# Kernel tuning notes

Hardware: AMD Instinct MI355X
Metric: run time of the kernel (lower is better)

Reference implementation:

```python
import jax, jax.numpy as jnp
import numpy as np

WS = 8      # window size
S = 2       # num_heads
GRID = jnp.linspace(-2.0, 2.0, 8)  # RBF grid, num_grids=8
DENOM = 4.0 / 7.0                  # (grid_max-grid_min)/(num_grids-1)


def _layernorm(x, g, b, eps=1e-5):
    mu = x.mean(-1, keepdims=True)
    var = ((x - mu) ** 2).mean(-1, keepdims=True)
    return (x - mu) * jax.lax.rsqrt(var + eps) * g + b


def _fastkan(x, ln_g, ln_b, ws, wb, bb):
    # x: (..., in_dim). RBF basis: (..., in_dim, 8) -> flatten -> spline GEMM; plus SiLU base path.
    ln = _layernorm(x, ln_g, ln_b)
    basis = jnp.exp(-(((ln[..., None] - GRID) / DENOM) ** 2))
    flat = basis.reshape(*basis.shape[:-2], -1)
    return flat @ ws.T + jax.nn.silu(x) @ wb.T + bb


def setup_inputs() -> dict:
    key = jax.random.key(0)
    ks = jax.random.split(key, 16)
    d = {
        'x': jax.random.normal(ks[0], (4, 32, 256, 256), dtype=jnp.float32),
        'pn_g': jnp.ones((32,), jnp.float32), 'pn_b': jnp.zeros((32,), jnp.float32),
        'k1_ln_g': jnp.ones((16,), jnp.float32), 'k1_ln_b': jnp.zeros((16,), jnp.float32),
        'k1_ws': jax.random.normal(ks[1], (16, 128), jnp.float32) * 0.1,
        'k1_wb': jax.random.normal(ks[2], (16, 16), jnp.float32) * 0.1,
        'k1_bb': jnp.zeros((16,), jnp.float32),
        'k2_ln_g': jnp.ones((16,), jnp.float32), 'k2_ln_b': jnp.zeros((16,), jnp.float32),
        'k2_ws': jax.random.normal(ks[3], (16, 128), jnp.float32) * 0.1,
        'k2_wb': jax.random.normal(ks[4], (16, 16), jnp.float32) * 0.1,
        'k2_bb': jnp.zeros((16,), jnp.float32),
        'k3_ln_g': jnp.ones((32,), jnp.float32), 'k3_ln_b': jnp.zeros((32,), jnp.float32),
        'k3_ws': jax.random.normal(ks[5], (32, 256), jnp.float32) * 0.1,
        'k3_wb': jax.random.normal(ks[6], (32, 32), jnp.float32) * 0.1,
        'k3_bb': jnp.zeros((32,), jnp.float32),
        'k4_ln_g': jnp.ones((32,), jnp.float32), 'k4_ln_b': jnp.zeros((32,), jnp.float32),
        'k4_ws': jax.random.normal(ks[7], (32, 256), jnp.float32) * 0.1,
        'k4_wb': jax.random.normal(ks[8], (32, 32), jnp.float32) * 0.1,
        'k4_bb': jnp.zeros((32,), jnp.float32),
    }
    return d


def reference(x, pn_g, pn_b,
              k1_ln_g, k1_ln_b, k1_ws, k1_wb, k1_bb,
              k2_ln_g, k2_ln_b, k2_ws, k2_wb, k2_bb,
              k3_ln_g, k3_ln_b, k3_ws, k3_wb, k3_bb,
              k4_ln_g, k4_ln_b, k4_ws, k4_wb, k4_bb):
    B, C, H, W = x.shape
    c = C // S
    # b c h w -> b h w c, then window partition (shift_size=0, no padding)
    xh = jnp.transpose(x, (0, 2, 3, 1))
    wins = xh.reshape(B, H // WS, WS, W // WS, WS, C).transpose(0, 1, 3, 2, 4, 5).reshape(-1, WS, WS, C)
    b = wins.shape[0]
    # PreNormResidual
    y = _layernorm(wins, pn_g, pn_b)
    # branch 1: 'b h w (c s) -> b (w c) (h s)'
    a = y.reshape(b, WS, WS, c, S).transpose(0, 2, 3, 1, 4).reshape(b, WS * c, WS * S)
    a = _fastkan(a, k1_ln_g, k1_ln_b, k1_ws, k1_wb, k1_bb)
    a = a.reshape(b, WS, c, WS, S).transpose(0, 3, 1, 2, 4).reshape(b, WS, WS, C)
    # branch 2: 'b h w (c s) -> b (h c) (w s)'
    d = y.reshape(b, WS, WS, c, S).transpose(0, 1, 3, 2, 4).reshape(b, WS * c, WS * S)
    d = _fastkan(d, k2_ln_g, k2_ln_b, k2_ws, k2_wb, k2_bb)
    d = d.reshape(b, WS, c, WS, S).transpose(0, 1, 3, 2, 4).reshape(b, WS, WS, C)
    # branch 3: channel mixing
    e = _fastkan(y.reshape(b, WS * WS, C), k3_ln_g, k3_ln_b, k3_ws, k3_wb, k3_bb).reshape(b, WS, WS, C)
    z = a + d + e
    # output KAN layer then residual
    z = _fastkan(z.reshape(b, WS * WS, C), k4_ln_g, k4_ln_b, k4_ws, k4_wb, k4_bb).reshape(b, WS, WS, C)
    out = z + wins
    # window reverse, back to b c h w
    out = out.reshape(B, H // WS, W // WS, WS, WS, C).transpose(0, 1, 3, 2, 4, 5).reshape(B, H, W, C)
    return jnp.transpose(out, (0, 3, 1, 2))
```

## Files before the change

kernel.cpp:

```cpp
#include <hip/hip_runtime.h>

typedef __attribute__((ext_vector_type(8))) short  s8v;
typedef __attribute__((ext_vector_type(8))) __bf16 b8v;
typedef __attribute__((ext_vector_type(4))) float  f4v;
typedef __attribute__((ext_vector_type(2))) float  f2v;

#define LDST 36
#define TBL_N 960

#define WAVE_FENCE() do { asm volatile("s_waitcnt lgkmcnt(0)" ::: "memory"); \
                          __builtin_amdgcn_sched_barrier(0); } while(0)

#define W2_OFF 2560
#define W3_OFF 5120
#define W4_OFF 14336
#define W_TOTAL 23552
#define PREP_TOTAL (192 + W_TOTAL)

__device__ __forceinline__ float frcp_(float x){ return __builtin_amdgcn_rcpf(x); }
__device__ __forceinline__ float rsq_(float x){ return __builtin_amdgcn_rsqf(x); }
__device__ __forceinline__ float silu_(float x){ return x * frcp_(1.0f + __expf(-x)); }

__device__ __forceinline__ s8v b2s(b8v v){ union { b8v b; s8v s; } u; u.b = v; return u.s; }

__device__ __forceinline__ void gl_lds16(const void* g, void* l){
  __builtin_amdgcn_global_load_lds(
      (const __attribute__((address_space(1))) unsigned int*)g,
      (__attribute__((address_space(3))) unsigned int*)l, 16, 0, 0);
}

__device__ __forceinline__ b8v basis8bf_(float u){
  float b = __expf(-u*u);
  float A = __expf(2.0f*u);
  b8v r;
  r[0] = (__bf16)b;
  b *= A * 0.36787944117144233f;   r[1] = (__bf16)b;
  b *= A * 0.049787068367863944f;  r[2] = (__bf16)b;
  b *= A * 0.006737946999085467f;  r[3] = (__bf16)b;
  b *= A * 0.0009118819655545162f; r[4] = (__bf16)b;
  b *= A * 1.2340980408667956e-4f; r[5] = (__bf16)b;
  b *= A * 1.670170079024566e-5f;  r[6] = (__bf16)b;
  b *= A * 2.2603294069810542e-6f; r[7] = (__bf16)b;
  return r;
}

__device__ __forceinline__ s8v blut_(const s8v* TBL, float u){
  float fi = __builtin_fmaf(u, 64.0f, 256.5f);
  fi = fminf(fmaxf(fi, 0.0f), 959.0f);
  return TBL[(int)fi];
}

__global__ void prep_w(const float* __restrict__ ws1, const float* __restrict__ wb1,
                       const float* __restrict__ ws2, const float* __restrict__ wb2,
                       const float* __restrict__ ws3, const float* __restrict__ wb3,
                       const float* __restrict__ ws4, const float* __restrict__ wb4,
                       const float* __restrict__ g1, const float* __restrict__ b1,
                       const float* __restrict__ g2, const float* __restrict__ b2,
                       const float* __restrict__ g3, const float* __restrict__ b3,
                       const float* __restrict__ g4, const float* __restrict__ b4,
                       float* __restrict__ LNP, __bf16* __restrict__ W){
  int idx = blockIdx.x*256 + threadIdx.x;
  if (idx >= PREP_TOTAL) return;
  if (idx < 192){
    float v;
    if      (idx < 16)  v = 1.75f * g1[idx];
    else if (idx < 32)  v = 1.75f * (b1[idx-16] + 2.0f);
    else if (idx < 48)  v = 1.75f * g2[idx-32];
    else if (idx < 64)  v = 1.75f * (b2[idx-48] + 2.0f);
    else if (idx < 96)  v = 1.75f * g3[idx-64];
    else if (idx < 128) v = 1.75f * (b3[idx-96] + 2.0f);
    else if (idx < 160) v = 1.75f * g4[idx-128];
    else                v = 1.75f * (b4[idx-160] + 2.0f);
    LNP[idx] = v;
    return;
  }
  int widx = idx - 192;
  float v;
  if (widx < W3_OFF){
    int base = (widx >= W2_OFF) ? W2_OFF : 0;
    const float* ws = base ? ws2 : ws1;
    const float* wb = base ? wb2 : wb1;
    int r = widx - base; int o = r/160, k = r%160;
    if (k < 128){
      int ks = k>>5, kg = (k>>3)&3, j = k&7;
      int elem = kg*4 + ks;
      v = ws[o*128 + elem*8 + j];
    } else {
      int kk = k-128; int kg = kk>>3, j = kk&7;
      v = (j<4) ? wb[o*16 + kg*4 + j] : 0.0f;
    }
  } else {
    int base = (widx >= W4_OFF) ? W4_OFF : W3_OFF;
    const float* ws = (base == W4_OFF) ? ws4 : ws3;
    const float* wb = (base == W4_OFF) ? wb4 : wb3;
    int r = widx - base; int o = r/288, k = r%288;
    if (k < 256){
      int ks = k>>5, kg = (k>>3)&3, j = k&7;
      int elem = kg*8 + ks;
      v = ws[o*256 + elem*8 + j];
    } else {
      int kk = k-256; int kg = kk>>3, j = kk&7;
      v = wb[o*32 + kg*8 + j];
    }
  }
  W[widx] = (__bf16)v;
}

__global__ __launch_bounds__(256,3)
void swin_kan_mfma(const float* __restrict__ x,
                   const float* __restrict__ pn_g, const float* __restrict__ pn_b,
                   const float* __restrict__ k1_bb, const float* __restrict__ k2_bb,
                   const float* __restrict__ k3_bb, const float* __restrict__ k4_bb,
                   const float* __restrict__ LNP,
                   const __bf16* __restrict__ Wbf,
                   float* __restrict__ out)
{
  __shared__ __attribute__((aligned(16))) float  yw[64][LDST];
  __shared__ __attribute__((aligned(16))) float  zA[64][LDST];
  __shared__ __attribute__((aligned(16))) float  LNPs[192];
  __shared__ __attribute__((aligned(16))) __bf16 W3s[9216];
  __shared__ __attribute__((aligned(16))) s8v    TBL[TBL_N];

  const int t   = threadIdx.x;
  const int bid = blockIdx.x;
  const int wid = (bid & 7)*512 + (bid >> 3);
  const int b   = wid >> 10;
  const int h0  = ((wid >> 5) & 31) * 8;
  const int w0  = (wid & 31) * 8;
  const int wave = t >> 6;
  const int lane = t & 63;
  const int fn = lane & 15, kg = lane >> 4;

  float4 xv0, xv1;

  {
    int ch = t & 31, h = t >> 5;
    const float* src = x + (((size_t)(b*32 + ch)*256 + (h0+h))*256 + w0);
    xv0 = *(const float4*)(src);
    xv1 = *(const float4*)(src + 4);
    int p = h*8;
    yw[p+0][ch]=xv0.x; yw[p+1][ch]=xv0.y; yw[p+2][ch]=xv0.z; yw[p+3][ch]=xv0.w;
    yw[p+4][ch]=xv1.x; yw[p+5][ch]=xv1.y; yw[p+6][ch]=xv1.z; yw[p+7][ch]=xv1.w;
    if (t < 192) LNPs[t] = LNP[t];
    const char* gsrc  = (const char*)(Wbf + W3_OFF);
    char*       lbase = (char*)W3s;
    for (int c = wave; c < 18; c += 4){
      gl_lds16(gsrc + c*1024 + lane*16, lbase + c*1024);
    }
    #pragma unroll
    for (int i = 0; i < 4; i++){
      int e = t + i*256;
      if (e < TBL_N){
        float u = -4.0f + (float)e * (1.0f/64.0f);
        TBL[e] = b2s(basis8bf_(u));
      }
    }
  }
  WAVE_FENCE();

  {
    int pos = t >> 2, part = t & 3;
    f4v a = *(const f4v*)&yw[pos][part*8];
    f4v c = *(const f4v*)&yw[pos][part*8+4];
    float s1 = a[0]+a[1]+a[2]+a[3]+c[0]+c[1]+c[2]+c[3];
    float s2 = a[0]*a[0]+a[1]*a[1]+a[2]*a[2]+a[3]*a[3]
             + c[0]*c[0]+c[1]*c[1]+c[2]*c[2]+c[3]*c[3];
    s1 += __shfl_xor(s1,1); s2 += __shfl_xor(s2,1);
    s1 += __shfl_xor(s1,2); s2 += __shfl_xor(s2,2);
    float mu  = s1*(1.0f/32.0f);
    float var = s2*(1.0f/32.0f) - mu*mu;
    float rs  = rsq_(var + 1e-5f);
    f4v g0 = *(const f4v*)&pn_g[part*8], g1 = *(const f4v*)&pn_g[part*8+4];
    f4v b0 = *(const f4v*)&pn_b[part*8], b1 = *(const f4v*)&pn_b[part*8+4];
    f4v o0, o1;
    #pragma unroll
    for (int j=0;j<4;j++){ o0[j] = (a[j]-mu)*rs*g0[j] + b0[j]; o1[j] = (c[j]-mu)*rs*g1[j] + b1[j]; }
    *(f4v*)&yw[pos][part*8]   = o0;
    *(f4v*)&yw[pos][part*8+4] = o1;
  }
  __syncthreads();

  {
    const bool br2 = (wave >= 2);
    const __bf16* Wp  = Wbf + (br2 ? W2_OFF : 0);
    const float* bbp = br2 ? k2_bb : k1_bb;
    const int gb = br2 ? 32 : 0, b2b = gb + 16;
    s8v wfr[5];
    #pragma unroll
    for (int ks=0;ks<5;ks++) wfr[ks] = *(const s8v*)&Wp[fn*160 + ks*32 + kg*8];
    f4v bias = *(const f4v*)&bbp[kg*4];
    f4v G  = *(const f4v*)&LNPs[gb  + kg*4];
    f4v B2 = *(const f4v*)&LNPs[b2b + kg*4];

    f2v va[4], vb[4];
    #pragma unroll
    for (int mi=0; mi<4; mi++){
      const int ck = (wave & 1)*4 + mi;
      const int posA = br2 ? (ck*8 + 2*kg) : ((2*kg)*8 + ck);
      const int posB = posA + (br2 ? 1 : 8);
      va[mi] = *(const f2v*)&yw[posA][2*fn];
      vb[mi] = *(const f2v*)&yw[posB][2*fn];
    }
    float mu4[4], rs4[4];
    #pragma unroll
    for (int mi=0; mi<4; mi++){
      float s1 = va[mi][0]+va[mi][1]+vb[mi][0]+vb[mi][1];
      float s2 = va[mi][0]*va[mi][0]+va[mi][1]*va[mi][1]+vb[mi][0]*vb[mi][0]+vb[mi][1]*vb[mi][1];
      s1 += __shfl_xor(s1,16); s2 += __shfl_xor(s2,16);
      s1 += __shfl_xor(s1,32); s2 += __shfl_xor(s2,32);
      float mu = s1*(1.0f/16.0f);
      mu4[mi] = mu;
      rs4[mi] = rsq_(s2*(1.0f/16.0f) - mu*mu + 1e-5f);
    }
    f4v accs[4];
    #pragma unroll
    for (int mi=0; mi<4; mi++){
      float v[4] = { va[mi][0], va[mi][1], vb[mi][0], vb[mi][1] };
      b8v bb = {};
      #pragma unroll
      for (int j=0;j<4;j++) bb[j] = (__bf16)silu_(v[j]);
      f4v acc = bias;
      #pragma unroll
      for (int ks=0;ks<4;ks++){
        float pp = G[ks]*rs4[mi];
        float qq = __builtin_fmaf(-mu4[mi], pp, B2[ks]);
        float u  = __builtin_fmaf(v[ks], pp, qq);
        acc = __builtin_amdgcn_mfma_f32_16x16x32_bf16(wfr[ks], blut_(TBL, u), acc, 0,0,0);
      }
      acc = __builtin_amdgcn_mfma_f32_16x16x32_bf16(wfr[4], b2s(bb), acc, 0,0,0);
      accs[mi] = acc;
    }

    if (!br2){
      #pragma unroll
      for (int mi=0; mi<4; mi++){
        const int ck = (wave & 1)*4 + mi;
        *(f2v*)&zA[(2*kg+0)*8 + ck][2*fn] = f2v{accs[mi][0], accs[mi][1]};
        *(f2v*)&zA[(2*kg+1)*8 + ck][2*fn] = f2v{accs[mi][2], accs[mi][3]};
      }
    }
    __syncthreads();
    if (br2){
      #pragma unroll
      for (int mi=0; mi<4; mi++){
        const int ck = (wave & 1)*4 + mi;
        f2v o0 = *(f2v*)&zA[ck*8 + 2*kg+0][2*fn];
        f2v o1 = *(f2v*)&zA[ck*8 + 2*kg+1][2*fn];
        o0[0] += accs[mi][0]; o0[1] += accs[mi][1];
        o1[0] += accs[mi][2]; o1[1] += accs[mi][3];
        *(f2v*)&zA[ck*8 + 2*kg+0][2*fn] = o0;
        *(f2v*)&zA[ck*8 + 2*kg+1][2*fn] = o1;
      }
    }
  }
  __syncthreads();

  {
    const int r = wave*16 + fn;
    f4v v0 = *(const f4v*)&yw[r][kg*8];
    f4v v1 = *(const f4v*)&yw[r][kg*8+4];
    float v[8] = { v0[0],v0[1],v0[2],v0[3], v1[0],v1[1],v1[2],v1[3] };
    b8v bb;
    #pragma unroll
    for (int ks=0;ks<8;ks++) bb[ks] = (__bf16)silu_(v[ks]);
    float s1=0.f, s2=0.f;
    #pragma unroll
    for (int ks=0;ks<8;ks++){ s1 += v[ks]; s2 += v[ks]*v[ks]; }
    s1 += __shfl_xor(s1,16); s2 += __shfl_xor(s2,16);
    s1 += __shfl_xor(s1,32); s2 += __shfl_xor(s2,32);
    float mu  = s1*(1.0f/32.0f);
    float var = s2*(1.0f/32.0f) - mu*mu;
    float rs  = rsq_(var + 1e-5f);

    f4v Ga = *(const f4v*)&LNPs[64 + kg*8], Gb = *(const f4v*)&LNPs[64 + kg*8 + 4];
    f4v Ba = *(const f4v*)&LNPs[96 + kg*8], Bb = *(const f4v*)&LNPs[96 + kg*8 + 4];
    float G8[8]  = { Ga[0],Ga[1],Ga[2],Ga[3], Gb[0],Gb[1],Gb[2],Gb[3] };
    float B8[8]  = { Ba[0],Ba[1],Ba[2],Ba[3], Bb[0],Bb[1],Bb[2],Bb[3] };

    f4v acc0 = *(const f4v*)&k3_bb[kg*4];
    f4v acc1 = *(const f4v*)&k3_bb[16 + kg*4];
    #pragma unroll
    for (int ks=0;ks<8;ks++){
      float pp = G8[ks]*rs;
      float qq = __builtin_fmaf(-mu, pp, B8[ks]);
      float u  = __builtin_fmaf(v[ks], pp, qq);
      s8v bf = blut_(TBL, u);
      s8v wa = *(const s8v*)&W3s[fn*288      + ks*32 + kg*8];
      s8v wb = *(const s8v*)&W3s[(16+fn)*288 + ks*32 + kg*8];
      acc0 = __builtin_amdgcn_mfma_f32_16x16x32_bf16(wa, bf, acc0, 0,0,0);
      acc1 = __builtin_amdgcn_mfma_f32_16x16x32_bf16(wb, bf, acc1, 0,0,0);
    }
    {
      s8v wa = *(const s8v*)&W3s[fn*288      + 256 + kg*8];
      s8v wb = *(const s8v*)&W3s[(16+fn)*288 + 256 + kg*8];
      acc0 = __builtin_amdgcn_mfma_f32_16x16x32_bf16(wa, b2s(bb), acc0, 0,0,0);
      acc1 = __builtin_amdgcn_mfma_f32_16x16x32_bf16(wb, b2s(bb), acc1, 0,0,0);
    }
    f4v za0 = *(const f4v*)&zA[r][kg*4];
    f4v za1 = *(const f4v*)&zA[r][16+kg*4];
    *(f4v*)&zA[r][kg*4]    = acc0 + za0;
    *(f4v*)&zA[r][16+kg*4] = acc1 + za1;
  }
  WAVE_FENCE();

  {
    const int r = wave*16 + fn;
    f4v v0 = *(const f4v*)&zA[r][kg*8];
    f4v v1 = *(const f4v*)&zA[r][kg*8+4];
    float v[8] = { v0[0],v0[1],v0[2],v0[3], v1[0],v1[1],v1[2],v1[3] };
    float s1=0.f, s2=0.f;
    #pragma unroll
    for (int ks=0;ks<8;ks++){ s1 += v[ks]; s2 += v[ks]*v[ks]; }
    s1 += __shfl_xor(s1,16); s2 += __shfl_xor(s2,16);
    s1 += __shfl_xor(s1,32); s2 += __shfl_xor(s2,32);
    float mu  = s1*(1.0f/32.0f);
    float var = s2*(1.0f/32.0f) - mu*mu;
    float rs  = rsq_(var + 1e-5f);

    f4v Ga = *(const f4v*)&LNPs[128 + kg*8], Gb = *(const f4v*)&LNPs[128 + kg*8 + 4];
    f4v Ba = *(const f4v*)&LNPs[160 + kg*8], Bb = *(const f4v*)&LNPs[160 + kg*8 + 4];
    float G8[8]  = { Ga[0],Ga[1],Ga[2],Ga[3], Gb[0],Gb[1],Gb[2],Gb[3] };
    float B8[8]  = { Ba[0],Ba[1],Ba[2],Ba[3], Bb[0],Bb[1],Bb[2],Bb[3] };

    f4v acc0 = *(const f4v*)&k4_bb[kg*4];
    f4v acc1 = *(const f4v*)&k4_bb[16 + kg*4];
    b8v bb;
    #pragma unroll
    for (int ks=0;ks<8;ks++){
      float pp = G8[ks]*rs;
      float qq = __builtin_fmaf(-mu, pp, B8[ks]);
      float u  = __builtin_fmaf(v[ks], pp, qq);
      s8v bf = blut_(TBL, u);
      s8v wa = *(const s8v*)&Wbf[W4_OFF + fn*288      + ks*32 + kg*8];
      s8v wb = *(const s8v*)&Wbf[W4_OFF + (16+fn)*288 + ks*32 + kg*8];
      acc0 = __builtin_amdgcn_mfma_f32_16x16x32_bf16(wa, bf, acc0, 0,0,0);
      acc1 = __builtin_amdgcn_mfma_f32_16x16x32_bf16(wb, bf, acc1, 0,0,0);
      bb[ks] = (__bf16)silu_(v[ks]);
    }
    {
      s8v wa = *(const s8v*)&Wbf[W4_OFF + fn*288      + 256 + kg*8];
      s8v wb = *(const s8v*)&Wbf[W4_OFF + (16+fn)*288 + 256 + kg*8];
      acc0 = __builtin_amdgcn_mfma_f32_16x16x32_bf16(wa, b2s(bb), acc0, 0,0,0);
      acc1 = __builtin_amdgcn_mfma_f32_16x16x32_bf16(wb, b2s(bb), acc1, 0,0,0);
    }
    *(f4v*)&yw[r][kg*4]    = acc0;
    *(f4v*)&yw[r][16+kg*4] = acc1;
  }
  WAVE_FENCE();

  {
    int ch = t & 31, h = t >> 5;
    const size_t base = (((size_t)(b*32 + ch)*256 + (h0+h))*256 + w0);
    int p = h*8;
    float4 v0 = { yw[p+0][ch]+xv0.x, yw[p+1][ch]+xv0.y, yw[p+2][ch]+xv0.z, yw[p+3][ch]+xv0.w };
    float4 v1 = { yw[p+4][ch]+xv1.x, yw[p+5][ch]+xv1.y, yw[p+6][ch]+xv1.z, yw[p+7][ch]+xv1.w };
    *(float4*)(out + base)     = v0;
    *(float4*)(out + base + 4) = v1;
  }
}

extern "C" void kernel_launch(void* const* d_in, const int* in_sizes, int n_in,
                              void* d_out, int out_size, void* d_ws, size_t ws_size,
                              hipStream_t stream) {
  const float* x      = (const float*)d_in[0];
  const float* pn_g   = (const float*)d_in[1];
  const float* pn_b   = (const float*)d_in[2];
  const float* k1_ln_g= (const float*)d_in[3];
  const float* k1_ln_b= (const float*)d_in[4];
  const float* k1_ws  = (const float*)d_in[5];
  const float* k1_wb  = (const float*)d_in[6];
  const float* k1_bb  = (const float*)d_in[7];
  const float* k2_ln_g= (const float*)d_in[8];
  const float* k2_ln_b= (const float*)d_in[9];
  const float* k2_ws  = (const float*)d_in[10];
  const float* k2_wb  = (const float*)d_in[11];
  const float* k2_bb  = (const float*)d_in[12];
  const float* k3_ln_g= (const float*)d_in[13];
  const float* k3_ln_b= (const float*)d_in[14];
  const float* k3_ws  = (const float*)d_in[15];
  const float* k3_wb  = (const float*)d_in[16];
  const float* k3_bb  = (const float*)d_in[17];
  const float* k4_ln_g= (const float*)d_in[18];
  const float* k4_ln_b= (const float*)d_in[19];
  const float* k4_ws  = (const float*)d_in[20];
  const float* k4_wb  = (const float*)d_in[21];
  const float* k4_bb  = (const float*)d_in[22];
  float* out = (float*)d_out;
  float*  LNP = (float*)d_ws;
  __bf16* Wbf = (__bf16*)((char*)d_ws + 768);

  hipLaunchKernelGGL(prep_w, dim3((PREP_TOTAL+255)/256), dim3(256), 0, stream,
                     k1_ws, k1_wb, k2_ws, k2_wb, k3_ws, k3_wb, k4_ws, k4_wb,
                     k1_ln_g, k1_ln_b, k2_ln_g, k2_ln_b,
                     k3_ln_g, k3_ln_b, k4_ln_g, k4_ln_b,
                     LNP, Wbf);

  hipLaunchKernelGGL(swin_kan_mfma, dim3(4096), dim3(256), 0, stream,
                     x, pn_g, pn_b,
                     k1_bb, k2_bb, k3_bb, k4_bb,
                     LNP, Wbf, out);
}
```

Baseline: 61.37 us.

## Process two windows per 512-thread block to amortize shared weight/table setup

Each block now handles two 8x8 windows with 512 threads, duplicating the per-window activation buffers while sharing the W3 weight staging and RBF lookup table across both windows. This halves the per-window cost of loading weights into LDS and building the basis table. In exchange, block-wide syncs now span twice as many waves, launch bounds change to 512x2, and LDS per block grows, which may change occupancy.

```diff
diff --git a/kernel.cpp b/kernel.cpp
--- a/kernel.cpp
+++ b/kernel.cpp
@@ -106,7 +106,7 @@
   W[widx] = (__bf16)v;
 }
 
-__global__ __launch_bounds__(256,3)
+__global__ __launch_bounds__(512,2)
 void swin_kan_mfma(const float* __restrict__ x,
                    const float* __restrict__ pn_g, const float* __restrict__ pn_b,
                    const float* __restrict__ k1_bb, const float* __restrict__ k2_bb,
@@ -115,41 +115,48 @@
                    const __bf16* __restrict__ Wbf,
                    float* __restrict__ out)
 {
-  __shared__ __attribute__((aligned(16))) float  yw[64][LDST];
-  __shared__ __attribute__((aligned(16))) float  zA[64][LDST];
+  __shared__ __attribute__((aligned(16))) float  yw[2][64][LDST];
+  __shared__ __attribute__((aligned(16))) float  zA[2][64][LDST];
   __shared__ __attribute__((aligned(16))) float  LNPs[192];
   __shared__ __attribute__((aligned(16))) __bf16 W3s[9216];
   __shared__ __attribute__((aligned(16))) s8v    TBL[TBL_N];
 
-  const int t   = threadIdx.x;
-  const int bid = blockIdx.x;
-  const int wid = (bid & 7)*512 + (bid >> 3);
-  const int b   = wid >> 10;
-  const int h0  = ((wid >> 5) & 31) * 8;
-  const int w0  = (wid & 31) * 8;
-  const int wave = t >> 6;
-  const int lane = t & 63;
+  const int t    = threadIdx.x;
+  const int win  = t >> 8;
+  const int tw   = t & 255;
+  const int bid  = blockIdx.x;
+  const int pair = (bid & 7)*256 + (bid >> 3);
+  const int wid  = pair*2 + win;
+  const int b    = wid >> 10;
+  const int h0   = ((wid >> 5) & 31) * 8;
+  const int w0   = (wid & 31) * 8;
+  const int wave = tw >> 6;
+  const int lane = tw & 63;
   const int fn = lane & 15, kg = lane >> 4;
 
+  float (*ywp)[LDST] = yw[win];
+  float (*zAp)[LDST] = zA[win];
+
   float4 xv0, xv1;
 
   {
-    int ch = t & 31, h = t >> 5;
+    int ch = tw & 31, h = tw >> 5;
     const float* src = x + (((size_t)(b*32 + ch)*256 + (h0+h))*256 + w0);
     xv0 = *(const float4*)(src);
     xv1 = *(const float4*)(src + 4);
     int p = h*8;
-    yw[p+0][ch]=xv0.x; yw[p+1][ch]=xv0.y; yw[p+2][ch]=xv0.z; yw[p+3][ch]=xv0.w;
-    yw[p+4][ch]=xv1.x; yw[p+5][ch]=xv1.y; yw[p+6][ch]=xv1.z; yw[p+7][ch]=xv1.w;
+    ywp[p+0][ch]=xv0.x; ywp[p+1][ch]=xv0.y; ywp[p+2][ch]=xv0.z; ywp[p+3][ch]=xv0.w;
+    ywp[p+4][ch]=xv1.x; ywp[p+5][ch]=xv1.y; ywp[p+6][ch]=xv1.z; ywp[p+7][ch]=xv1.w;
     if (t < 192) LNPs[t] = LNP[t];
+    const int waveAll = t >> 6;
     const char* gsrc  = (const char*)(Wbf + W3_OFF);
     char*       lbase = (char*)W3s;
-    for (int c = wave; c < 18; c += 4){
+    for (int c = waveAll; c < 18; c += 8){
       gl_lds16(gsrc + c*1024 + lane*16, lbase + c*1024);
     }
     #pragma unroll
-    for (int i = 0; i < 4; i++){
-      int e = t + i*256;
+    for (int i = 0; i < 2; i++){
+      int e = t + i*512;
       if (e < TBL_N){
         float u = -4.0f + (float)e * (1.0f/64.0f);
         TBL[e] = b2s(basis8bf_(u));
@@ -159,9 +166,9 @@
   WAVE_FENCE();
 
   {
-    int pos = t >> 2, part = t & 3;
-    f4v a = *(const f4v*)&yw[pos][part*8];
-    f4v c = *(const f4v*)&yw[pos][part*8+4];
+    int pos = tw >> 2, part = tw & 3;
+    f4v a = *(const f4v*)&ywp[pos][part*8];
+    f4v c = *(const f4v*)&ywp[pos][part*8+4];
     float s1 = a[0]+a[1]+a[2]+a[3]+c[0]+c[1]+c[2]+c[3];
     float s2 = a[0]*a[0]+a[1]*a[1]+a[2]*a[2]+a[3]*a[3]
              + c[0]*c[0]+c[1]*c[1]+c[2]*c[2]+c[3]*c[3];
@@ -175,13 +182,13 @@
     f4v o0, o1;
     #pragma unroll
     for (int j=0;j<4;j++){ o0[j] = (a[j]-mu)*rs*g0[j] + b0[j]; o1[j] = (c[j]-mu)*rs*g1[j] + b1[j]; }
-    *(f4v*)&yw[pos][part*8]   = o0;
-    *(f4v*)&yw[pos][part*8+4] = o1;
+    *(f4v*)&ywp[pos][part*8]   = o0;
+    *(f4v*)&ywp[pos][part*8+4] = o1;
   }
   __syncthreads();
 
   {
-    const bool br2 = (wave >= 2);
+    const bool br2 = (tw >= 128);
     const __bf16* Wp  = Wbf + (br2 ? W2_OFF : 0);
     const float* bbp = br2 ? k2_bb : k1_bb;
     const int gb = br2 ? 32 : 0, b2b = gb + 16;
@@ -198,8 +205,8 @@
       const int ck = (wave & 1)*4 + mi;
       const int posA = br2 ? (ck*8 + 2*kg) : ((2*kg)*8 + ck);
       const int posB = posA + (br2 ? 1 : 8);
-      va[mi] = *(const f2v*)&yw[posA][2*fn];
-      vb[mi] = *(const f2v*)&yw[posB][2*fn];
+      va[mi] = *(const f2v*)&ywp[posA][2*fn];
+      vb[mi] = *(const f2v*)&ywp[posB][2*fn];
     }
     float mu4[4], rs4[4];
     #pragma unroll
@@ -235,8 +242,8 @@
       #pragma unroll
       for (int mi=0; mi<4; mi++){
         const int ck = (wave & 1)*4 + mi;
-        *(f2v*)&zA[(2*kg+0)*8 + ck][2*fn] = f2v{accs[mi][0], accs[mi][1]};
-        *(f2v*)&zA[(2*kg+1)*8 + ck][2*fn] = f2v{accs[mi][2], accs[mi][3]};
+        *(f2v*)&zAp[(2*kg+0)*8 + ck][2*fn] = f2v{accs[mi][0], accs[mi][1]};
+        *(f2v*)&zAp[(2*kg+1)*8 + ck][2*fn] = f2v{accs[mi][2], accs[mi][3]};
       }
     }
     __syncthreads();
@@ -244,12 +251,12 @@
       #pragma unroll
       for (int mi=0; mi<4; mi++){
         const int ck = (wave & 1)*4 + mi;
-        f2v o0 = *(f2v*)&zA[ck*8 + 2*kg+0][2*fn];
-        f2v o1 = *(f2v*)&zA[ck*8 + 2*kg+1][2*fn];
+        f2v o0 = *(f2v*)&zAp[ck*8 + 2*kg+0][2*fn];
+        f2v o1 = *(f2v*)&zAp[ck*8 + 2*kg+1][2*fn];
         o0[0] += accs[mi][0]; o0[1] += accs[mi][1];
         o1[0] += accs[mi][2]; o1[1] += accs[mi][3];
-        *(f2v*)&zA[ck*8 + 2*kg+0][2*fn] = o0;
-        *(f2v*)&zA[ck*8 + 2*kg+1][2*fn] = o1;
+        *(f2v*)&zAp[ck*8 + 2*kg+0][2*fn] = o0;
+        *(f2v*)&zAp[ck*8 + 2*kg+1][2*fn] = o1;
       }
     }
   }
@@ -257,8 +264,8 @@
 
   {
     const int r = wave*16 + fn;
-    f4v v0 = *(const f4v*)&yw[r][kg*8];
-    f4v v1 = *(const f4v*)&yw[r][kg*8+4];
+    f4v v0 = *(const f4v*)&ywp[r][kg*8];
+    f4v v1 = *(const f4v*)&ywp[r][kg*8+4];
     float v[8] = { v0[0],v0[1],v0[2],v0[3], v1[0],v1[1],v1[2],v1[3] };
     b8v bb;
     #pragma unroll
@@ -296,17 +303,17 @@
       acc0 = __builtin_amdgcn_mfma_f32_16x16x32_bf16(wa, b2s(bb), acc0, 0,0,0);
       acc1 = __builtin_amdgcn_mfma_f32_16x16x32_bf16(wb, b2s(bb), acc1, 0,0,0);
     }
-    f4v za0 = *(const f4v*)&zA[r][kg*4];
-    f4v za1 = *(const f4v*)&zA[r][16+kg*4];
-    *(f4v*)&zA[r][kg*4]    = acc0 + za0;
-    *(f4v*)&zA[r][16+kg*4] = acc1 + za1;
+    f4v za0 = *(const f4v*)&zAp[r][kg*4];
+    f4v za1 = *(const f4v*)&zAp[r][16+kg*4];
+    *(f4v*)&zAp[r][kg*4]    = acc0 + za0;
+    *(f4v*)&zAp[r][16+kg*4] = acc1 + za1;
   }
   WAVE_FENCE();
 
   {
     const int r = wave*16 + fn;
-    f4v v0 = *(const f4v*)&zA[r][kg*8];
-    f4v v1 = *(const f4v*)&zA[r][kg*8+4];
+    f4v v0 = *(const f4v*)&zAp[r][kg*8];
+    f4v v1 = *(const f4v*)&zAp[r][kg*8+4];
     float v[8] = { v0[0],v0[1],v0[2],v0[3], v1[0],v1[1],v1[2],v1[3] };
     float s1=0.f, s2=0.f;
     #pragma unroll
@@ -343,17 +350,17 @@
       acc0 = __builtin_amdgcn_mfma_f32_16x16x32_bf16(wa, b2s(bb), acc0, 0,0,0);
       acc1 = __builtin_amdgcn_mfma_f32_16x16x32_bf16(wb, b2s(bb), acc1, 0,0,0);
     }
-    *(f4v*)&yw[r][kg*4]    = acc0;
-    *(f4v*)&yw[r][16+kg*4] = acc1;
+    *(f4v*)&ywp[r][kg*4]    = acc0;
+    *(f4v*)&ywp[r][16+kg*4] = acc1;
   }
   WAVE_FENCE();
 
   {
-    int ch = t & 31, h = t >> 5;
+    int ch = tw & 31, h = tw >> 5;
     const size_t base = (((size_t)(b*32 + ch)*256 + (h0+h))*256 + w0);
     int p = h*8;
-    float4 v0 = { yw[p+0][ch]+xv0.x, yw[p+1][ch]+xv0.y, yw[p+2][ch]+xv0.z, yw[p+3][ch]+xv0.w };
-    float4 v1 = { yw[p+4][ch]+xv1.x, yw[p+5][ch]+xv1.y, yw[p+6][ch]+xv1.z, yw[p+7][ch]+xv1.w };
+    float4 v0 = { ywp[p+0][ch]+xv0.x, ywp[p+1][ch]+xv0.y, ywp[p+2][ch]+xv0.z, ywp[p+3][ch]+xv0.w };
+    float4 v1 = { ywp[p+4][ch]+xv1.x, ywp[p+5][ch]+xv1.y, ywp[p+6][ch]+xv1.z, ywp[p+7][ch]+xv1.w };
     *(float4*)(out + base)     = v0;
     *(float4*)(out + base + 4) = v1;
   }
@@ -395,7 +402,7 @@
                      k3_ln_g, k3_ln_b, k4_ln_g, k4_ln_b,
                      LNP, Wbf);
 
-  hipLaunchKernelGGL(swin_kan_mfma, dim3(4096), dim3(256), 0, stream,
+  hipLaunchKernelGGL(swin_kan_mfma, dim3(2048), dim3(512), 0, stream,
                      x, pn_g, pn_b,
                      k1_bb, k2_bb, k3_bb, k4_bb,
                      LNP, Wbf, out);
```

Result: no change. 61.69 us (+0.5%).

## Process two windows per block to amortize per-block setup

Applied to the files above, without the earlier changes.

Each block now handles two 8x8 windows instead of one, halving the grid to 2048 blocks. The per-block W3 weight staging into LDS, the RBF lookup-table build, the LN parameter loads and the register-held weight fragments are now reused across both windows. In exchange the yw/zA LDS buffers double, register pressure rises, and launch bounds drop to 2 blocks per CU, which lowers occupancy and latency hiding.

```diff
diff --git a/kernel.cpp b/kernel.cpp
--- a/kernel.cpp
+++ b/kernel.cpp
@@ -106,7 +106,7 @@
   W[widx] = (__bf16)v;
 }
 
-__global__ __launch_bounds__(256,3)
+__global__ __launch_bounds__(256,2)
 void swin_kan_mfma(const float* __restrict__ x,
                    const float* __restrict__ pn_g, const float* __restrict__ pn_b,
                    const float* __restrict__ k1_bb, const float* __restrict__ k2_bb,
@@ -115,32 +115,41 @@
                    const __bf16* __restrict__ Wbf,
                    float* __restrict__ out)
 {
-  __shared__ __attribute__((aligned(16))) float  yw[64][LDST];
-  __shared__ __attribute__((aligned(16))) float  zA[64][LDST];
+  __shared__ __attribute__((aligned(16))) float  yw[2][64][LDST];
+  __shared__ __attribute__((aligned(16))) float  zA[2][64][LDST];
   __shared__ __attribute__((aligned(16))) float  LNPs[192];
   __shared__ __attribute__((aligned(16))) __bf16 W3s[9216];
   __shared__ __attribute__((aligned(16))) s8v    TBL[TBL_N];
 
-  const int t   = threadIdx.x;
-  const int bid = blockIdx.x;
-  const int wid = (bid & 7)*512 + (bid >> 3);
-  const int b   = wid >> 10;
-  const int h0  = ((wid >> 5) & 31) * 8;
-  const int w0  = (wid & 31) * 8;
+  const int t    = threadIdx.x;
+  const int bid  = blockIdx.x;
+  const int pair = (bid & 7)*256 + (bid >> 3);
   const int wave = t >> 6;
   const int lane = t & 63;
   const int fn = lane & 15, kg = lane >> 4;
 
-  float4 xv0, xv1;
+  int bW[2], h0W[2], w0W[2];
+  #pragma unroll
+  for (int W=0; W<2; W++){
+    int wid = pair*2 + W;
+    bW[W]  = wid >> 10;
+    h0W[W] = ((wid >> 5) & 31) * 8;
+    w0W[W] = (wid & 31) * 8;
+  }
+
+  float4 rx0[2], rx1[2];
 
   {
     int ch = t & 31, h = t >> 5;
-    const float* src = x + (((size_t)(b*32 + ch)*256 + (h0+h))*256 + w0);
-    xv0 = *(const float4*)(src);
-    xv1 = *(const float4*)(src + 4);
-    int p = h*8;
-    yw[p+0][ch]=xv0.x; yw[p+1][ch]=xv0.y; yw[p+2][ch]=xv0.z; yw[p+3][ch]=xv0.w;
-    yw[p+4][ch]=xv1.x; yw[p+5][ch]=xv1.y; yw[p+6][ch]=xv1.z; yw[p+7][ch]=xv1.w;
+    #pragma unroll
+    for (int W=0; W<2; W++){
+      const float* src = x + (((size_t)(bW[W]*32 + ch)*256 + (h0W[W]+h))*256 + w0W[W]);
+      rx0[W] = *(const float4*)(src);
+      rx1[W] = *(const float4*)(src + 4);
+      int p = h*8;
+      yw[W][p+0][ch]=rx0[W].x; yw[W][p+1][ch]=rx0[W].y; yw[W][p+2][ch]=rx0[W].z; yw[W][p+3][ch]=rx0[W].w;
+      yw[W][p+4][ch]=rx1[W].x; yw[W][p+5][ch]=rx1[W].y; yw[W][p+6][ch]=rx1[W].z; yw[W][p+7][ch]=rx1[W].w;
+    }
     if (t < 192) LNPs[t] = LNP[t];
     const char* gsrc  = (const char*)(Wbf + W3_OFF);
     char*       lbase = (char*)W3s;
@@ -160,23 +169,26 @@
 
   {
     int pos = t >> 2, part = t & 3;
-    f4v a = *(const f4v*)&yw[pos][part*8];
-    f4v c = *(const f4v*)&yw[pos][part*8+4];
-    float s1 = a[0]+a[1]+a[2]+a[3]+c[0]+c[1]+c[2]+c[3];
-    float s2 = a[0]*a[0]+a[1]*a[1]+a[2]*a[2]+a[3]*a[3]
-             + c[0]*c[0]+c[1]*c[1]+c[2]*c[2]+c[3]*c[3];
-    s1 += __shfl_xor(s1,1); s2 += __shfl_xor(s2,1);
-    s1 += __shfl_xor(s1,2); s2 += __shfl_xor(s2,2);
-    float mu  = s1*(1.0f/32.0f);
-    float var = s2*(1.0f/32.0f) - mu*mu;
-    float rs  = rsq_(var + 1e-5f);
-    f4v g0 = *(const f4v*)&pn_g[part*8], g1 = *(const f4v*)&pn_g[part*8+4];
-    f4v b0 = *(const f4v*)&pn_b[part*8], b1 = *(const f4v*)&pn_b[part*8+4];
-    f4v o0, o1;
-    #pragma unroll
-    for (int j=0;j<4;j++){ o0[j] = (a[j]-mu)*rs*g0[j] + b0[j]; o1[j] = (c[j]-mu)*rs*g1[j] + b1[j]; }
-    *(f4v*)&yw[pos][part*8]   = o0;
-    *(f4v*)&yw[pos][part*8+4] = o1;
+    #pragma unroll
+    for (int W=0; W<2; W++){
+      f4v a = *(const f4v*)&yw[W][pos][part*8];
+      f4v c = *(const f4v*)&yw[W][pos][part*8+4];
+      float s1 = a[0]+a[1]+a[2]+a[3]+c[0]+c[1]+c[2]+c[3];
+      float s2 = a[0]*a[0]+a[1]*a[1]+a[2]*a[2]+a[3]*a[3]
+               + c[0]*c[0]+c[1]*c[1]+c[2]*c[2]+c[3]*c[3];
+      s1 += __shfl_xor(s1,1); s2 += __shfl_xor(s2,1);
+      s1 += __shfl_xor(s1,2); s2 += __shfl_xor(s2,2);
+      float mu  = s1*(1.0f/32.0f);
+      float var = s2*(1.0f/32.0f) - mu*mu;
+      float rs  = rsq_(var + 1e-5f);
+      f4v g0 = *(const f4v*)&pn_g[part*8], g1 = *(const f4v*)&pn_g[part*8+4];
+      f4v b0 = *(const f4v*)&pn_b[part*8], b1 = *(const f4v*)&pn_b[part*8+4];
+      f4v o0, o1;
+      #pragma unroll
+      for (int j=0;j<4;j++){ o0[j] = (a[j]-mu)*rs*g0[j] + b0[j]; o1[j] = (c[j]-mu)*rs*g1[j] + b1[j]; }
+      *(f4v*)&yw[W][pos][part*8]   = o0;
+      *(f4v*)&yw[W][pos][part*8+4] = o1;
+    }
   }
   __syncthreads();
 
@@ -192,64 +204,73 @@
     f4v G  = *(const f4v*)&LNPs[gb  + kg*4];
     f4v B2 = *(const f4v*)&LNPs[b2b + kg*4];
 
-    f2v va[4], vb[4];
-    #pragma unroll
-    for (int mi=0; mi<4; mi++){
-      const int ck = (wave & 1)*4 + mi;
-      const int posA = br2 ? (ck*8 + 2*kg) : ((2*kg)*8 + ck);
-      const int posB = posA + (br2 ? 1 : 8);
-      va[mi] = *(const f2v*)&yw[posA][2*fn];
-      vb[mi] = *(const f2v*)&yw[posB][2*fn];
-    }
-    float mu4[4], rs4[4];
-    #pragma unroll
-    for (int mi=0; mi<4; mi++){
-      float s1 = va[mi][0]+va[mi][1]+vb[mi][0]+vb[mi][1];
-      float s2 = va[mi][0]*va[mi][0]+va[mi][1]*va[mi][1]+vb[mi][0]*vb[mi][0]+vb[mi][1]*vb[mi][1];
-      s1 += __shfl_xor(s1,16); s2 += __shfl_xor(s2,16);
-      s1 += __shfl_xor(s1,32); s2 += __shfl_xor(s2,32);
-      float mu = s1*(1.0f/16.0f);
-      mu4[mi] = mu;
-      rs4[mi] = rsq_(s2*(1.0f/16.0f) - mu*mu + 1e-5f);
-    }
-    f4v accs[4];
-    #pragma unroll
-    for (int mi=0; mi<4; mi++){
-      float v[4] = { va[mi][0], va[mi][1], vb[mi][0], vb[mi][1] };
-      b8v bb = {};
-      #pragma unroll
-      for (int j=0;j<4;j++) bb[j] = (__bf16)silu_(v[j]);
-      f4v acc = bias;
-      #pragma unroll
-      for (int ks=0;ks<4;ks++){
-        float pp = G[ks]*rs4[mi];
-        float qq = __builtin_fmaf(-mu4[mi], pp, B2[ks]);
-        float u  = __builtin_fmaf(v[ks], pp, qq);
-        acc = __builtin_amdgcn_mfma_f32_16x16x32_bf16(wfr[ks], blut_(TBL, u), acc, 0,0,0);
-      }
-      acc = __builtin_amdgcn_mfma_f32_16x16x32_bf16(wfr[4], b2s(bb), acc, 0,0,0);
-      accs[mi] = acc;
-    }
-
-    if (!br2){
+    f4v accs[2][4];
+    #pragma unroll
+    for (int W=0; W<2; W++){
+      f2v va[4], vb[4];
       #pragma unroll
       for (int mi=0; mi<4; mi++){
         const int ck = (wave & 1)*4 + mi;
-        *(f2v*)&zA[(2*kg+0)*8 + ck][2*fn] = f2v{accs[mi][0], accs[mi][1]};
-        *(f2v*)&zA[(2*kg+1)*8 + ck][2*fn] = f2v{accs[mi][2], accs[mi][3]};
+        const int posA = br2 ? (ck*8 + 2*kg) : ((2*kg)*8 + ck);
+        const int posB = posA + (br2 ? 1 : 8);
+        va[mi] = *(const f2v*)&yw[W][posA][2*fn];
+        vb[mi] = *(const f2v*)&yw[W][posB][2*fn];
+      }
+      float mu4[4], rs4[4];
+      #pragma unroll
+      for (int mi=0; mi<4; mi++){
+        float s1 = va[mi][0]+va[mi][1]+vb[mi][0]+vb[mi][1];
+        float s2 = va[mi][0]*va[mi][0]+va[mi][1]*va[mi][1]+vb[mi][0]*vb[mi][0]+vb[mi][1]*vb[mi][1];
+        s1 += __shfl_xor(s1,16); s2 += __shfl_xor(s2,16);
+        s1 += __shfl_xor(s1,32); s2 += __shfl_xor(s2,32);
+        float mu = s1*(1.0f/16.0f);
+        mu4[mi] = mu;
+        rs4[mi] = rsq_(s2*(1.0f/16.0f) - mu*mu + 1e-5f);
+      }
+      #pragma unroll
+      for (int mi=0; mi<4; mi++){
+        float v[4] = { va[mi][0], va[mi][1], vb[mi][0], vb[mi][1] };
+        b8v bb = {};
+        #pragma unroll
+        for (int j=0;j<4;j++) bb[j] = (__bf16)silu_(v[j]);
+        f4v acc = bias;
+        #pragma unroll
+        for (int ks=0;ks<4;ks++){
+          float pp = G[ks]*rs4[mi];
+          float qq = __builtin_fmaf(-mu4[mi], pp, B2[ks]);
+          float u  = __builtin_fmaf(v[ks], pp, qq);
+          acc = __builtin_amdgcn_mfma_f32_16x16x32_bf16(wfr[ks], blut_(TBL, u), acc, 0,0,0);
+        }
+        acc = __builtin_amdgcn_mfma_f32_16x16x32_bf16(wfr[4], b2s(bb), acc, 0,0,0);
+        accs[W][mi] = acc;
+      }
+    }
+
+    if (!br2){
+      #pragma unroll
+      for (int W=0; W<2; W++){
+        #pragma unroll
+        for (int mi=0; mi<4; mi++){
+          const int ck = (wave & 1)*4 + mi;
+          *(f2v*)&zA[W][(2*kg+0)*8 + ck][2*fn] = f2v{accs[W][mi][0], accs[W][mi][1]};
+          *(f2v*)&zA[W][(2*kg+1)*8 + ck][2*fn] = f2v{accs[W][mi][2], accs[W][mi][3]};
+        }
       }
     }
     __syncthreads();
     if (br2){
       #pragma unroll
-      for (int mi=0; mi<4; mi++){
-        const int ck = (wave & 1)*4 + mi;
-        f2v o0 = *(f2v*)&zA[ck*8 + 2*kg+0][2*fn];
-        f2v o1 = *(f2v*)&zA[ck*8 + 2*kg+1][2*fn];
-        o0[0] += accs[mi][0]; o0[1] += accs[mi][1];
-        o1[0] += accs[mi][2]; o1[1] += accs[mi][3];
-        *(f2v*)&zA[ck*8 + 2*kg+0][2*fn] = o0;
-        *(f2v*)&zA[ck*8 + 2*kg+1][2*fn] = o1;
+      for (int W=0; W<2; W++){
+        #pragma unroll
+        for (int mi=0; mi<4; mi++){
+          const int ck = (wave & 1)*4 + mi;
+          f2v o0 = *(f2v*)&zA[W][ck*8 + 2*kg+0][2*fn];
+          f2v o1 = *(f2v*)&zA[W][ck*8 + 2*kg+1][2*fn];
+          o0[0] += accs[W][mi][0]; o0[1] += accs[W][mi][1];
+          o1[0] += accs[W][mi][2]; o1[1] += accs[W][mi][3];
+          *(f2v*)&zA[W][ck*8 + 2*kg+0][2*fn] = o0;
+          *(f2v*)&zA[W][ck*8 + 2*kg+1][2*fn] = o1;
+        }
       }
     }
   }
@@ -257,105 +278,118 @@
 
   {
     const int r = wave*16 + fn;
-    f4v v0 = *(const f4v*)&yw[r][kg*8];
-    f4v v1 = *(const f4v*)&yw[r][kg*8+4];
-    float v[8] = { v0[0],v0[1],v0[2],v0[3], v1[0],v1[1],v1[2],v1[3] };
-    b8v bb;
-    #pragma unroll
-    for (int ks=0;ks<8;ks++) bb[ks] = (__bf16)silu_(v[ks]);
-    float s1=0.f, s2=0.f;
-    #pragma unroll
-    for (int ks=0;ks<8;ks++){ s1 += v[ks]; s2 += v[ks]*v[ks]; }
-    s1 += __shfl_xor(s1,16); s2 += __shfl_xor(s2,16);
-    s1 += __shfl_xor(s1,32); s2 += __shfl_xor(s2,32);
-    float mu  = s1*(1.0f/32.0f);
-    float var = s2*(1.0f/32.0f) - mu*mu;
-    float rs  = rsq_(var + 1e-5f);
-
     f4v Ga = *(const f4v*)&LNPs[64 + kg*8], Gb = *(const f4v*)&LNPs[64 + kg*8 + 4];
     f4v Ba = *(const f4v*)&LNPs[96 + kg*8], Bb = *(const f4v*)&LNPs[96 + kg*8 + 4];
     float G8[8]  = { Ga[0],Ga[1],Ga[2],Ga[3], Gb[0],Gb[1],Gb[2],Gb[3] };
     float B8[8]  = { Ba[0],Ba[1],Ba[2],Ba[3], Bb[0],Bb[1],Bb[2],Bb[3] };
-
-    f4v acc0 = *(const f4v*)&k3_bb[kg*4];
-    f4v acc1 = *(const f4v*)&k3_bb[16 + kg*4];
-    #pragma unroll
-    for (int ks=0;ks<8;ks++){
-      float pp = G8[ks]*rs;
-      float qq = __builtin_fmaf(-mu, pp, B8[ks]);
-      float u  = __builtin_fmaf(v[ks], pp, qq);
-      s8v bf = blut_(TBL, u);
-      s8v wa = *(const s8v*)&W3s[fn*288      + ks*32 + kg*8];
-      s8v wb = *(const s8v*)&W3s[(16+fn)*288 + ks*32 + kg*8];
-      acc0 = __builtin_amdgcn_mfma_f32_16x16x32_bf16(wa, bf, acc0, 0,0,0);
-      acc1 = __builtin_amdgcn_mfma_f32_16x16x32_bf16(wb, bf, acc1, 0,0,0);
-    }
-    {
-      s8v wa = *(const s8v*)&W3s[fn*288      + 256 + kg*8];
-      s8v wb = *(const s8v*)&W3s[(16+fn)*288 + 256 + kg*8];
-      acc0 = __builtin_amdgcn_mfma_f32_16x16x32_bf16(wa, b2s(bb), acc0, 0,0,0);
-      acc1 = __builtin_amdgcn_mfma_f32_16x16x32_bf16(wb, b2s(bb), acc1, 0,0,0);
-    }
-    f4v za0 = *(const f4v*)&zA[r][kg*4];
-    f4v za1 = *(const f4v*)&zA[r][16+kg*4];
-    *(f4v*)&zA[r][kg*4]    = acc0 + za0;
-    *(f4v*)&zA[r][16+kg*4] = acc1 + za1;
+    f4v bias0 = *(const f4v*)&k3_bb[kg*4];
+    f4v bias1 = *(const f4v*)&k3_bb[16 + kg*4];
+
+    #pragma unroll
+    for (int W=0; W<2; W++){
+      f4v v0 = *(const f4v*)&yw[W][r][kg*8];
+      f4v v1 = *(const f4v*)&yw[W][r][kg*8+4];
+      float v[8] = { v0[0],v0[1],v0[2],v0[3], v1[0],v1[1],v1[2],v1[3] };
+      b8v bb;
+      #pragma unroll
+      for (int ks=0;ks<8;ks++) bb[ks] = (__bf16)silu_(v[ks]);
+      float s1=0.f, s2=0.f;
+      #pragma unroll
+      for (int ks=0;ks<8;ks++){ s1 += v[ks]; s2 += v[ks]*v[ks]; }
+      s1 += __shfl_xor(s1,16); s2 += __shfl_xor(s2,16);
+      s1 += __shfl_xor(s1,32); s2 += __shfl_xor(s2,32);
+      float mu  = s1*(1.0f/32.0f);
+      float var = s2*(1.0f/32.0f) - mu*mu;
+      float rs  = rsq_(var + 1e-5f);
+
+      f4v acc0 = bias0, acc1 = bias1;
+      #pragma unroll
+      for (int ks=0;ks<8;ks++){
+        float pp = G8[ks]*rs;
+        float qq = __builtin_fmaf(-mu, pp, B8[ks]);
+        float u  = __builtin_fmaf(v[ks], pp, qq);
+        s8v bf = blut_(TBL, u);
+        s8v wa = *(const s8v*)&W3s[fn*288      + ks*32 + kg*8];
+        s8v wb = *(const s8v*)&W3s[(16+fn)*288 + ks*32 + kg*8];
+        acc0 = __builtin_amdgcn_mfma_f32_16x16x32_bf16(wa, bf, acc0, 0,0,0);
+        acc1 = __builtin_amdgcn_mfma_f32_16x16x32_bf16(wb, bf, acc1, 0,0,0);
+      }
+      {
+        s8v wa = *(const s8v*)&W3s[fn*288      + 256 + kg*8];
+        s8v wb = *(const s8v*)&W3s[(16+fn)*288 + 256 + kg*8];
+        acc0 = __builtin_amdgcn_mfma_f32_16x16x32_bf16(wa, b2s(bb), acc0, 0,0,0);
+        acc1 = __builtin_amdgcn_mfma_f32_16x16x32_bf16(wb, b2s(bb), acc1, 0,0,0);
+      }
+      f4v za0 = *(const f4v*)&zA[W][r][kg*4];
+      f4v za1 = *(const f4v*)&zA[W][r][16+kg*4];
+      *(f4v*)&zA[W][r][kg*4]    = acc0 + za0;
+      *(f4v*)&zA[W][r][16+kg*4] = acc1 + za1;
+    }
   }
   WAVE_FENCE();
 
   {
     const int r = wave*16 + fn;
-    f4v v0 = *(const f4v*)&zA[r][kg*8];
-    f4v v1 = *(const f4v*)&zA[r][kg*8+4];
-    float v[8] = { v0[0],v0[1],v0[2],v0[3], v1[0],v1[1],v1[2],v1[3] };
-    float s1=0.f, s2=0.f;
-    #pragma unroll
-    for (int ks=0;ks<8;ks++){ s1 += v[ks]; s2 += v[ks]*v[ks]; }
-    s1 += __shfl_xor(s1,16); s2 += __shfl_xor(s2,16);
-    s1 += __shfl_xor(s1,32); s2 += __shfl_xor(s2,32);
-    float mu  = s1*(1.0f/32.0f);
-    float var = s2*(1.0f/32.0f) - mu*mu;
-    float rs  = rsq_(var + 1e-5f);
-
     f4v Ga = *(const f4v*)&LNPs[128 + kg*8], Gb = *(const f4v*)&LNPs[128 + kg*8 + 4];
     f4v Ba = *(const f4v*)&LNPs[160 + kg*8], Bb = *(const f4v*)&LNPs[160 + kg*8 + 4];
     float G8[8]  = { Ga[0],Ga[1],Ga[2],Ga[3], Gb[0],Gb[1],Gb[2],Gb[3] };
     float B8[8]  = { Ba[0],Ba[1],Ba[2],Ba[3], Bb[0],Bb[1],Bb[2],Bb[3] };
-
-    f4v acc0 = *(const f4v*)&k4_bb[kg*4];
-    f4v acc1 = *(const f4v*)&k4_bb[16 + kg*4];
-    b8v bb;
-    #pragma unroll
-    for (int ks=0;ks<8;ks++){
-      float pp = G8[ks]*rs;
-      float qq = __builtin_fmaf(-mu, pp, B8[ks]);
-      float u  = __builtin_fmaf(v[ks], pp, qq);
-      s8v bf = blut_(TBL, u);
-      s8v wa = *(const s8v*)&Wbf[W4_OFF + fn*288      + ks*32 + kg*8];
-      s8v wb = *(const s8v*)&Wbf[W4_OFF + (16+fn)*288 + ks*32 + kg*8];
-      acc0 = __builtin_amdgcn_mfma_f32_16x16x32_bf16(wa, bf, acc0, 0,0,0);
-      acc1 = __builtin_amdgcn_mfma_f32_16x16x32_bf16(wb, bf, acc1, 0,0,0);
-      bb[ks] = (__bf16)silu_(v[ks]);
-    }
-    {
-      s8v wa = *(const s8v*)&Wbf[W4_OFF + fn*288      + 256 + kg*8];
-      s8v wb = *(const s8v*)&Wbf[W4_OFF + (16+fn)*288 + 256 + kg*8];
-      acc0 = __builtin_amdgcn_mfma_f32_16x16x32_bf16(wa, b2s(bb), acc0, 0,0,0);
-      acc1 = __builtin_amdgcn_mfma_f32_16x16x32_bf16(wb, b2s(bb), acc1, 0,0,0);
-    }
-    *(f4v*)&yw[r][kg*4]    = acc0;
-    *(f4v*)&yw[r][16+kg*4] = acc1;
+    f4v bias0 = *(const f4v*)&k4_bb[kg*4];
+    f4v bias1 = *(const f4v*)&k4_bb[16 + kg*4];
+
+    #pragma unroll
+    for (int W=0; W<2; W++){
+      f4v v0 = *(const f4v*)&zA[W][r][kg*8];
+      f4v v1 = *(const f4v*)&zA[W][r][kg*8+4];
+      float v[8] = { v0[0],v0[1],v0[2],v0[3], v1[0],v1[1],v1[2],v1[3] };
+      float s1=0.f, s2=0.f;
+      #pragma unroll
+      for (int ks=0;ks<8;ks++){ s1 += v[ks]; s2 += v[ks]*v[ks]; }
+      s1 += __shfl_xor(s1,16); s2 += __shfl_xor(s2,16);
+      s1 += __shfl_xor(s1,32); s2 += __shfl_xor(s2,32);
+      float mu  = s1*(1.0f/32.0f);
+      float var = s2*(1.0f/32.0f) - mu*mu;
+      float rs  = rsq_(var + 1e-5f);
+
+      f4v acc0 = bias0, acc1 = bias1;
+      b8v bb;
+      #pragma unroll
+      for (int ks=0;ks<8;ks++){
+        float pp = G8[ks]*rs;
+        float qq = __builtin_fmaf(-mu, pp, B8[ks]);
+        float u  = __builtin_fmaf(v[ks], pp, qq);
+        s8v bf = blut_(TBL, u);
+        s8v wa = *(const s8v*)&Wbf[W4_OFF + fn*288      + ks*32 + kg*8];
+        s8v wb = *(const s8v*)&Wbf[W4_OFF + (16+fn)*288 + ks*32 + kg*8];
+        acc0 = __builtin_amdgcn_mfma_f32_16x16x32_bf16(wa, bf, acc0, 0,0,0);
+        acc1 = __builtin_amdgcn_mfma_f32_16x16x32_bf16(wb, bf, acc1, 0,0,0);
+        bb[ks] = (__bf16)silu_(v[ks]);
+      }
+      {
+        s8v wa = *(const s8v*)&Wbf[W4_OFF + fn*288      + 256 + kg*8];
+        s8v wb = *(const s8v*)&Wbf[W4_OFF + (16+fn)*288 + 256 + kg*8];
+        acc0 = __builtin_amdgcn_mfma_f32_16x16x32_bf16(wa, b2s(bb), acc0, 0,0,0);
+        acc1 = __builtin_amdgcn_mfma_f32_16x16x32_bf16(wb, b2s(bb), acc1, 0,0,0);
+      }
+      *(f4v*)&yw[W][r][kg*4]    = acc0;
+      *(f4v*)&yw[W][r][16+kg*4] = acc1;
+    }
   }
   WAVE_FENCE();
 
   {
     int ch = t & 31, h = t >> 5;
-    const size_t base = (((size_t)(b*32 + ch)*256 + (h0+h))*256 + w0);
     int p = h*8;
-    float4 v0 = { yw[p+0][ch]+xv0.x, yw[p+1][ch]+xv0.y, yw[p+2][ch]+xv0.z, yw[p+3][ch]+xv0.w };
-    float4 v1 = { yw[p+4][ch]+xv1.x, yw[p+5][ch]+xv1.y, yw[p+6][ch]+xv1.z, yw[p+7][ch]+xv1.w };
-    *(float4*)(out + base)     = v0;
-    *(float4*)(out + base + 4) = v1;
+    #pragma unroll
+    for (int W=0; W<2; W++){
+      const size_t base = (((size_t)(bW[W]*32 + ch)*256 + (h0W[W]+h))*256 + w0W[W]);
+      float4 v0 = { yw[W][p+0][ch]+rx0[W].x, yw[W][p+1][ch]+rx0[W].y,
+                    yw[W][p+2][ch]+rx0[W].z, yw[W][p+3][ch]+rx0[W].w };
+      float4 v1 = { yw[W][p+4][ch]+rx1[W].x, yw[W][p+5][ch]+rx1[W].y,
+                    yw[W][p+6][ch]+rx1[W].z, yw[W][p+7][ch]+rx1[W].w };
+      *(float4*)(out + base)     = v0;
+      *(float4*)(out + base + 4) = v1;
+    }
   }
 }
 
@@ -395,7 +429,7 @@
                      k3_ln_g, k3_ln_b, k4_ln_g, k4_ln_b,
                      LNP, Wbf);
 
-  hipLaunchKernelGGL(swin_kan_mfma, dim3(4096), dim3(256), 0, stream,
+  hipLaunchKernelGGL(swin_kan_mfma, dim3(2048), dim3(256), 0, stream,
                      x, pn_g, pn_b,
                      k1_bb, k2_bb, k3_bb, k4_bb,
                      LNP, Wbf, out);
```

Result: no change. 62.18 us (+1.3%).
